# Kernel tuning notes

Hardware: AMD Instinct MI355X
Metric: run time of the kernel (lower is better)

Reference implementation:

```python
import jax, jax.numpy as jnp
import numpy as np
from jax import lax

D_MODEL = 32
N_HEADS = 8
QS = 24       # query_shape
FLANGE = 8    # memory_flange


def _conv3x3(x, w, b=None):
    y = lax.conv_general_dilated(x, w, (1, 1), 'SAME',
                                 dimension_numbers=('NCHW', 'OIHW', 'NCHW'))
    if b is not None:
        y = y + b[None, :, None, None]
    return y


def _forward(x, q_w, q_b, k_w, k_b, v_w, v_b, out_w):
    B, Cin, H, W0 = x.shape
    nh, dm, qs, fl = N_HEADS, D_MODEL, QS, FLANGE
    c = dm // nh  # depth per head (=4)

    q = _conv3x3(x, q_w, q_b)
    k = _conv3x3(x, k_w, k_b)
    v = _conv3x3(x, v_w, v_b)

    pad = (-W0) % qs
    if pad:
        p = ((0, 0), (0, 0), (0, 0), (0, pad))
        q = jnp.pad(q, p); k = jnp.pad(k, p); v = jnp.pad(v, p)
    T = q.shape[-1]
    M = T // qs
    F = 2 * fl + qs  # window length (=40)

    q = q.reshape(B, nh, c, H, T) * (c ** -0.5)
    k = jnp.pad(k.reshape(B, nh, c, H, T), ((0, 0),) * 4 + ((fl, fl),))
    v = jnp.pad(v.reshape(B, nh, c, H, T), ((0, 0),) * 4 + ((fl, fl),))

    # Faithful reproduction of torch.as_strided(k, shape, unfold_q.stride()):
    # the source uses q's (contiguous, time-length T) strides on k/v whose
    # storage rows have length T+2*fl, so we gather by storage-linear index.
    s0, s1, s2, s3 = nh * c * H * T, c * H * T, H * T, T
    idx = (jnp.arange(B)[:, None, None, None, None, None] * s0
           + jnp.arange(nh)[:, None, None, None, None] * s1
           + jnp.arange(c)[:, None, None, None] * s2
           + jnp.arange(H)[:, None, None] * s3
           + jnp.arange(M)[:, None] * qs
           + jnp.arange(F))  # (B,nh,c,H,M,F)
    uk = k.reshape(-1)[idx]
    uv = v.reshape(-1)[idx]

    qq = q.reshape(B, nh, c, H, M, qs).transpose(0, 1, 4, 3, 5, 2)
    qq = qq.reshape(B * nh * M, H * qs, c)                     # (G, H*qs, c)
    k2 = uk.transpose(0, 1, 4, 2, 3, 5).reshape(B * nh * M, c, H * F)
    v2 = uv.transpose(0, 1, 4, 3, 5, 2).reshape(B * nh * M, H * F, c)

    # note: source uses -1e-09 (not -1e9); reproduced exactly
    bias = (jnp.sum(jnp.abs(k2), axis=-2, keepdims=True) == 0).astype(k2.dtype) * (-1e-09)
    weights = jax.nn.softmax(qq @ k2 + bias, axis=-1)
    o = weights @ v2                                            # (G, H*qs, c)

    o = o.reshape(B, nh, M, H, qs, c).transpose(0, 1, 5, 3, 2, 4)
    o = o.reshape(B, dm, H, M * qs)[..., :H, :W0]
    return _conv3x3(o, out_w)


def setup_inputs() -> dict:
    key = jax.random.key(0)
    ks = jax.random.split(key, 8)
    B, Cin, H, W = 2, 64, 32, 192
    s = 0.05
    return {
        'x': jax.random.normal(ks[0], (B, Cin, H, W), jnp.float32),
        'q_w': jax.random.normal(ks[1], (D_MODEL, Cin, 3, 3), jnp.float32) * s,
        'q_b': jax.random.normal(ks[2], (D_MODEL,), jnp.float32) * s,
        'k_w': jax.random.normal(ks[3], (D_MODEL, Cin, 3, 3), jnp.float32) * s,
        'k_b': jax.random.normal(ks[4], (D_MODEL,), jnp.float32) * s,
        'v_w': jax.random.normal(ks[5], (D_MODEL, Cin, 3, 3), jnp.float32) * s,
        'v_b': jax.random.normal(ks[6], (D_MODEL,), jnp.float32) * s,
        'out_w': jax.random.normal(ks[7], (64, D_MODEL, 3, 3), jnp.float32) * s,
    }


def reference(x, q_w, q_b, k_w, k_b, v_w, v_b, out_w):
    return _forward(x, q_w, q_b, k_w, k_b, v_w, v_b, out_w)
```

## Files before the change

kernel.cpp:

```cpp
#include <hip/hip_runtime.h>

namespace {
constexpr int B   = 2;
constexpr int CIN = 64;
constexpr int H   = 32;
constexpr int W   = 192;
constexpr int DM  = 32;
constexpr int NH  = 8;
constexpr int C   = 4;
constexpr int QS  = 24;
constexpr int FL  = 8;
constexpr int T   = 192;
constexpr int TP  = T + 2 * FL;
constexpr int M   = T / QS;
constexpr int F   = 2 * FL + QS;
constexpr int HF  = H * F;
constexpr int JC  = HF / 4;
constexpr int WP  = 196;
constexpr int HWP = H * WP;

constexpr size_t XP_OFF  = 0;
constexpr size_t KVI_OFF = 0;
constexpr size_t Q_OFF   = 1310720;
constexpr size_t K_OFF   = Q_OFF + 393216;
constexpr size_t V_OFF   = K_OFF + 425984;
constexpr size_t O_OFF   = K_OFF;
constexpr size_t ZR_OFF  = V_OFF + 425984;

constexpr int S0 = NH * C * H * T;
constexpr int S1 = C * H * T;
constexpr int S2 = H * T;
constexpr int S3 = T;
}

__global__ __launch_bounds__(256) void prep_k(const float* __restrict__ x,
                                              float* __restrict__ ws) {
  int bid = blockIdx.x;
  int tid = threadIdx.x;
  if (bid < 4096) {
    if (tid < WP) {
      float v = (tid >= 1 && tid <= W) ? x[(size_t)bid * W + (tid - 1)] : 0.f;
      ws[XP_OFF + (size_t)bid * WP + tid] = v;
    }
  } else if (bid < 4224) {
    int t = (bid - 4096) * 256 + tid;
    int row = t >> 4;
    int p = t & 15;
    int col = (p < 8) ? p : (192 + p);
    size_t addr = (size_t)row * TP + col;
    ws[K_OFF + addr] = 0.f;
    ws[V_OFF + addr] = 0.f;
  } else {
    ws[ZR_OFF + tid] = 0.f;
  }
}

__global__ __launch_bounds__(192) void qkv_conv_k(
    const float* __restrict__ qw, const float* __restrict__ qb,
    const float* __restrict__ kw, const float* __restrict__ kb,
    const float* __restrict__ vw, const float* __restrict__ vb,
    float* __restrict__ ws) {
  int bid = blockIdx.x;
  int yq = bid & 7;
  int co = (bid >> 3) & 31;
  int b  = bid >> 8;
  int tid = threadIdx.x;
  int yl = tid / 48;
  int xq = tid - yl * 48;
  int y  = yq * 4 + yl;
  int xp = xq * 4;

  const float* zr  = ws + ZR_OFF;
  const float* xpb = ws + XP_OFF + (size_t)b * CIN * HWP;

  const float* p0 = (y > 0)     ? xpb + (y - 1) * WP + xp : zr + xp;
  const float* p1 = xpb + y * WP + xp;
  const float* p2 = (y < H - 1) ? xpb + (y + 1) * WP + xp : zr + xp;
  int st0 = (y > 0)     ? HWP : 0;
  int st2 = (y < H - 1) ? HWP : 0;

  const float* wq = qw + co * (CIN * 9);
  const float* wk = kw + co * (CIN * 9);
  const float* wv = vw + co * (CIN * 9);

  float q0b = qb[co], k0b = kb[co], v0b = vb[co];
  float Aq[4] = {q0b, q0b, q0b, q0b};
  float Ak[4] = {k0b, k0b, k0b, k0b};
  float Av[4] = {v0b, v0b, v0b, v0b};

#pragma unroll 2
  for (int ci = 0; ci < CIN; ++ci) {
    float4 a4 = *reinterpret_cast<const float4*>(p0);
    float2 a2 = *reinterpret_cast<const float2*>(p0 + 4);
    float4 b4 = *reinterpret_cast<const float4*>(p1);
    float2 b2 = *reinterpret_cast<const float2*>(p1 + 4);
    float4 c4 = *reinterpret_cast<const float4*>(p2);
    float2 c2 = *reinterpret_cast<const float2*>(p2 + 4);
    float av_[6] = {a4.x, a4.y, a4.z, a4.w, a2.x, a2.y};
    float bv_[6] = {b4.x, b4.y, b4.z, b4.w, b2.x, b2.y};
    float cv_[6] = {c4.x, c4.y, c4.z, c4.w, c2.x, c2.y};
#pragma unroll
    for (int dx = 0; dx < 3; ++dx) {
      float wq0 = wq[dx], wq1 = wq[3 + dx], wq2 = wq[6 + dx];
      float wk0 = wk[dx], wk1 = wk[3 + dx], wk2 = wk[6 + dx];
      float wv0 = wv[dx], wv1 = wv[3 + dx], wv2 = wv[6 + dx];
#pragma unroll
      for (int o = 0; o < 4; ++o) {
        float xa = av_[o + dx], xb = bv_[o + dx], xc = cv_[o + dx];
        Aq[o] = fmaf(xa, wq0, Aq[o]); Aq[o] = fmaf(xb, wq1, Aq[o]); Aq[o] = fmaf(xc, wq2, Aq[o]);
        Ak[o] = fmaf(xa, wk0, Ak[o]); Ak[o] = fmaf(xb, wk1, Ak[o]); Ak[o] = fmaf(xc, wk2, Ak[o]);
        Av[o] = fmaf(xa, wv0, Av[o]); Av[o] = fmaf(xb, wv1, Av[o]); Av[o] = fmaf(xc, wv2, Av[o]);
      }
    }
    p0 += st0; p1 += HWP; p2 += st2;
    wq += 9; wk += 9; wv += 9;
  }

  *reinterpret_cast<float4*>(ws + Q_OFF + ((size_t)(b * DM + co) * H + y) * T + xp) =
      make_float4(Aq[0], Aq[1], Aq[2], Aq[3]);
  int h = co >> 2, c4i = co & 3;
  size_t pa = ((size_t)((b * NH + h) * C + c4i) * H + y) * TP + FL + xp;
  *reinterpret_cast<float4*>(ws + K_OFF + pa) = make_float4(Ak[0], Ak[1], Ak[2], Ak[3]);
  *reinterpret_cast<float4*>(ws + V_OFF + pa) = make_float4(Av[0], Av[1], Av[2], Av[3]);
}

__global__ __launch_bounds__(256) void build_kv_k(float* __restrict__ ws) {
  const float* kp = ws + K_OFF;
  const float* vp = ws + V_OFF;
  float* kvi = ws + KVI_OFF;
  int t = blockIdx.x * 256 + threadIdx.x;
  int c  = t & 7;
  int gj = t >> 3;
  int g  = gj / HF;
  int j  = gj - g * HF;
  int b = g >> 6, h = (g >> 3) & 7, m = g & 7;
  int hh = j / F, f = j - hh * F;
  int ci = c & 3;
  const float* src = (c < 4) ? kp : vp;
  int addr = b * S0 + h * S1 + ci * S2 + hh * S3 + m * QS + f;
  kvi[t] = src[addr];
}

__global__ __launch_bounds__(256) void attn_k(float* __restrict__ ws) {
  const float* qbuf = ws + Q_OFF;
  const float* kvi  = ws + KVI_OFF;
  float*       ob   = ws + O_OFF;

  int g  = blockIdx.x;
  int rb = blockIdx.y;
  int b = g >> 6, h = (g >> 3) & 7, m = g & 7;
  int tid = threadIdx.x;
  int row = tid & 63;
  int jc  = __builtin_amdgcn_readfirstlane(tid >> 6);

  int r  = rb * 64 + row;
  int hh = r / QS, qi = r - hh * QS;
  size_t qidx = (((size_t)(b * DM + h * C) * H + hh) * T) + m * QS + qi;
  float q0 = qbuf[qidx]             * 0.5f;
  float q1 = qbuf[qidx + H * T]     * 0.5f;
  float q2 = qbuf[qidx + 2 * H * T] * 0.5f;
  float q3 = qbuf[qidx + 3 * H * T] * 0.5f;

  const float* kvp = kvi + ((size_t)g * HF + (size_t)jc * JC) * 8;

  float s = 0.f, o0 = 0.f, o1 = 0.f, o2 = 0.f, o3 = 0.f;
#pragma unroll 4
  for (int j = 0; j < JC; ++j) {
    float4 k4 = *reinterpret_cast<const float4*>(kvp + j * 8);
    float4 v4 = *reinterpret_cast<const float4*>(kvp + j * 8 + 4);
    float l = fmaf(q0, k4.x, fmaf(q1, k4.y, fmaf(q2, k4.z, q3 * k4.w)));
    float e = __expf(l);
    s += e;
    o0 = fmaf(e, v4.x, o0);
    o1 = fmaf(e, v4.y, o1);
    o2 = fmaf(e, v4.z, o2);
    o3 = fmaf(e, v4.w, o3);
  }

  __shared__ float red[4][64][5];
  red[jc][row][0] = s;
  red[jc][row][1] = o0;
  red[jc][row][2] = o1;
  red[jc][row][3] = o2;
  red[jc][row][4] = o3;
  __syncthreads();

  if (tid < 64) {
    float S = 0.f, O0 = 0.f, O1 = 0.f, O2 = 0.f, O3 = 0.f;
#pragma unroll
    for (int cx = 0; cx < 4; ++cx) {
      S  += red[cx][tid][0];
      O0 += red[cx][tid][1];
      O1 += red[cx][tid][2];
      O2 += red[cx][tid][3];
      O3 += red[cx][tid][4];
    }
    float inv = 1.0f / S;
    size_t obase = (((size_t)(b * DM + h * C) * H + hh) * WP) + 1 + m * QS + qi;
    ob[obase]            = O0 * inv;
    ob[obase + HWP]      = O1 * inv;
    ob[obase + 2 * HWP]  = O2 * inv;
    ob[obase + 3 * HWP]  = O3 * inv;
    if (m == 0 && qi == 0) {
      ob[obase - 1] = 0.f; ob[obase - 1 + HWP] = 0.f;
      ob[obase - 1 + 2 * HWP] = 0.f; ob[obase - 1 + 3 * HWP] = 0.f;
    }
    if (m == M - 1 && qi == QS - 1) {
      ob[obase + 1] = 0.f; ob[obase + 1 + HWP] = 0.f;
      ob[obase + 1 + 2 * HWP] = 0.f; ob[obase + 1 + 3 * HWP] = 0.f;
    }
  }
}

__global__ __launch_bounds__(192) void out_conv_k(const float* __restrict__ ws,
                                                  const float* __restrict__ ow,
                                                  float* __restrict__ out) {
  int bid = blockIdx.x;
  int yq = bid & 7;
  int cp = (bid >> 3) & 31;
  int b  = bid >> 8;
  int tid = threadIdx.x;
  int yl = tid / 48;
  int xq = tid - yl * 48;
  int y  = yq * 4 + yl;
  int xp = xq * 4;

  const float* zr  = ws + ZR_OFF;
  const float* obb = ws + O_OFF + (size_t)b * DM * HWP;

  const float* p0 = (y > 0)     ? obb + (y - 1) * WP + xp : zr + xp;
  const float* p1 = obb + y * WP + xp;
  const float* p2 = (y < H - 1) ? obb + (y + 1) * WP + xp : zr + xp;
  int st0 = (y > 0)     ? HWP : 0;
  int st2 = (y < H - 1) ? HWP : 0;

  int co0 = cp * 2;
  const float* w0 = ow + (size_t)co0 * (DM * 9);
  const float* w1 = w0 + DM * 9;
  float A0[4] = {0.f, 0.f, 0.f, 0.f};
  float A1[4] = {0.f, 0.f, 0.f, 0.f};

#pragma unroll 2
  for (int ci = 0; ci < DM; ++ci) {
    float4 a4 = *reinterpret_cast<const float4*>(p0);
    float2 a2 = *reinterpret_cast<const float2*>(p0 + 4);
    float4 b4 = *reinterpret_cast<const float4*>(p1);
    float2 b2 = *reinterpret_cast<const float2*>(p1 + 4);
    float4 c4 = *reinterpret_cast<const float4*>(p2);
    float2 c2 = *reinterpret_cast<const float2*>(p2 + 4);
    float av_[6] = {a4.x, a4.y, a4.z, a4.w, a2.x, a2.y};
    float bv_[6] = {b4.x, b4.y, b4.z, b4.w, b2.x, b2.y};
    float cv_[6] = {c4.x, c4.y, c4.z, c4.w, c2.x, c2.y};
#pragma unroll
    for (int dx = 0; dx < 3; ++dx) {
      float u0 = w0[dx], u1 = w0[3 + dx], u2 = w0[6 + dx];
      float t0 = w1[dx], t1 = w1[3 + dx], t2 = w1[6 + dx];
#pragma unroll
      for (int o = 0; o < 4; ++o) {
        float xa = av_[o + dx], xb = bv_[o + dx], xc = cv_[o + dx];
        A0[o] = fmaf(xa, u0, A0[o]); A0[o] = fmaf(xb, u1, A0[o]); A0[o] = fmaf(xc, u2, A0[o]);
        A1[o] = fmaf(xa, t0, A1[o]); A1[o] = fmaf(xb, t1, A1[o]); A1[o] = fmaf(xc, t2, A1[o]);
      }
    }
    p0 += st0; p1 += HWP; p2 += st2;
    w0 += 9; w1 += 9;
  }

  size_t ob0 = ((size_t)(b * 64 + co0) * H + y) * W + xp;
  *reinterpret_cast<float4*>(out + ob0)         = make_float4(A0[0], A0[1], A0[2], A0[3]);
  *reinterpret_cast<float4*>(out + ob0 + H * W) = make_float4(A1[0], A1[1], A1[2], A1[3]);
}

extern "C" void kernel_launch(void* const* d_in, const int* in_sizes, int n_in,
                              void* d_out, int out_size, void* d_ws, size_t ws_size,
                              hipStream_t stream) {
  const float* x  = (const float*)d_in[0];
  const float* qw = (const float*)d_in[1];
  const float* qb = (const float*)d_in[2];
  const float* kw = (const float*)d_in[3];
  const float* kb = (const float*)d_in[4];
  const float* vw = (const float*)d_in[5];
  const float* vb = (const float*)d_in[6];
  const float* ow = (const float*)d_in[7];
  float* out = (float*)d_out;
  float* ws  = (float*)d_ws;

  hipLaunchKernelGGL(prep_k,     dim3(4225), dim3(256), 0, stream, x, ws);
  hipLaunchKernelGGL(qkv_conv_k, dim3(512),  dim3(192), 0, stream,
                     qw, qb, kw, kb, vw, vb, ws);
  hipLaunchKernelGGL(build_kv_k, dim3(5120), dim3(256), 0, stream, ws);
  hipLaunchKernelGGL(attn_k,     dim3(128, 12), dim3(256), 0, stream, ws);
  hipLaunchKernelGGL(out_conv_k, dim3(512),  dim3(192), 0, stream, ws, ow, out);
}
```

Baseline: 100.3 us.

## Compute attention logits with fp16 MFMA and repack Q/K/V layouts

Replaces the scalar per-thread QK dot products with 16x16x32 fp16 MFMA instructions. Q and K are packed into fp16 tiles by new pack kernels, and V is stored transposed per channel in fp32. The cross-wave shared-memory reduction is removed; partial sums are instead combined with cross-lane shuffles inside each wave. The cost is an extra launch and fp16 rounding of logits. The MFMA input is mostly zero-padded, because only a depth of 4 is used out of 32.

```diff
diff --git a/kernel.cpp b/kernel.cpp
--- a/kernel.cpp
+++ b/kernel.cpp
@@ -1,4 +1,8 @@
 #include <hip/hip_runtime.h>
+
+typedef _Float16 f16;
+typedef __attribute__((ext_vector_type(8))) _Float16 f16x8;
+typedef __attribute__((ext_vector_type(4))) float f32x4;
 
 namespace {
 constexpr int B   = 2;
@@ -15,22 +19,29 @@
 constexpr int M   = T / QS;
 constexpr int F   = 2 * FL + QS;
 constexpr int HF  = H * F;
-constexpr int JC  = HF / 4;
 constexpr int WP  = 196;
 constexpr int HWP = H * WP;
 
-constexpr size_t XP_OFF  = 0;
-constexpr size_t KVI_OFF = 0;
-constexpr size_t Q_OFF   = 1310720;
-constexpr size_t K_OFF   = Q_OFF + 393216;
-constexpr size_t V_OFF   = K_OFF + 425984;
-constexpr size_t O_OFF   = K_OFF;
-constexpr size_t ZR_OFF  = V_OFF + 425984;
+constexpr size_t KVIK_OFF = 0;
+constexpr size_t QT_OFF   = 327680;
+constexpr size_t VT_OFF   = 524288;
+constexpr size_t XP_OFF   = 0;
+constexpr size_t Q_OFF    = 802816;
+constexpr size_t K_OFF    = 1196032;
+constexpr size_t V_OFF    = 1622016;
+constexpr size_t O_OFF    = K_OFF;
+constexpr size_t ZR_OFF   = 2048000;
 
 constexpr int S0 = NH * C * H * T;
 constexpr int S1 = C * H * T;
 constexpr int S2 = H * T;
 constexpr int S3 = T;
+}
+
+__device__ inline unsigned pk16rn(float a, float b) {
+  union { f16 h[2]; unsigned u; } c;
+  c.h[0] = (f16)a; c.h[1] = (f16)b;
+  return c.u;
 }
 
 __global__ __launch_bounds__(256) void prep_k(const float* __restrict__ x,
@@ -124,92 +135,115 @@
   *reinterpret_cast<float4*>(ws + V_OFF + pa) = make_float4(Av[0], Av[1], Av[2], Av[3]);
 }
 
-__global__ __launch_bounds__(256) void build_kv_k(float* __restrict__ ws) {
+__global__ __launch_bounds__(256) void pack_q_k(float* __restrict__ ws) {
+  int t = blockIdx.x * 256 + threadIdx.x;
+  int g = t / 768, row = t - g * 768;
+  int b = g >> 6, h = (g >> 3) & 7, m = g & 7;
+  int hh = row / QS, qi = row - hh * QS;
+  const float* qb = ws + Q_OFF;
+  size_t qidx = ((size_t)(b * DM + h * C) * H + hh) * T + m * QS + qi;
+  const float SC = 0.5f;
+  uint2 o;
+  o.x = pk16rn(qb[qidx] * SC,             qb[qidx + H * T] * SC);
+  o.y = pk16rn(qb[qidx + 2 * H * T] * SC, qb[qidx + 3 * H * T] * SC);
+  reinterpret_cast<uint2*>(ws + QT_OFF)[t] = o;
+}
+
+__global__ __launch_bounds__(256) void pack_kv_k(float* __restrict__ ws) {
+  int t = blockIdx.x * 256 + threadIdx.x;
+  int g = t / HF, key = t - g * HF;
+  int b = g >> 6, h = (g >> 3) & 7, m = g & 7;
+  int hh = key / F, f = key - hh * F;
+  int base = b * S0 + h * S1 + hh * S3 + m * QS + f;
   const float* kp = ws + K_OFF;
   const float* vp = ws + V_OFF;
-  float* kvi = ws + KVI_OFF;
-  int t = blockIdx.x * 256 + threadIdx.x;
-  int c  = t & 7;
-  int gj = t >> 3;
-  int g  = gj / HF;
-  int j  = gj - g * HF;
+  float k0 = kp[base], k1 = kp[base + S2], k2 = kp[base + 2 * S2], k3 = kp[base + 3 * S2];
+  float v0 = vp[base], v1 = vp[base + S2], v2 = vp[base + 2 * S2], v3 = vp[base + 3 * S2];
+  uint2 o; o.x = pk16rn(k0, k1); o.y = pk16rn(k2, k3);
+  reinterpret_cast<uint2*>(ws + KVIK_OFF)[t] = o;
+  float* vt = ws + VT_OFF;
+  size_t vg = (size_t)g * 4 * HF;
+  vt[vg + key]          = v0;
+  vt[vg + HF + key]     = v1;
+  vt[vg + 2 * HF + key] = v2;
+  vt[vg + 3 * HF + key] = v3;
+}
+
+__global__ __launch_bounds__(256) void attn_k(float* __restrict__ ws) {
+  const uint2* kvik = reinterpret_cast<const uint2*>(ws + KVIK_OFF);
+  const uint2* qt   = reinterpret_cast<const uint2*>(ws + QT_OFF);
+  const float* vt   = ws + VT_OFF;
+  float* ob = ws + O_OFF;
+
+  int g   = blockIdx.x;
+  int rb  = blockIdx.y;
   int b = g >> 6, h = (g >> 3) & 7, m = g & 7;
-  int hh = j / F, f = j - hh * F;
-  int ci = c & 3;
-  const float* src = (c < 4) ? kp : vp;
-  int addr = b * S0 + h * S1 + ci * S2 + hh * S3 + m * QS + f;
-  kvi[t] = src[addr];
-}
-
-__global__ __launch_bounds__(256) void attn_k(float* __restrict__ ws) {
-  const float* qbuf = ws + Q_OFF;
-  const float* kvi  = ws + KVI_OFF;
-  float*       ob   = ws + O_OFF;
-
-  int g  = blockIdx.x;
-  int rb = blockIdx.y;
-  int b = g >> 6, h = (g >> 3) & 7, m = g & 7;
-  int tid = threadIdx.x;
-  int row = tid & 63;
-  int jc  = __builtin_amdgcn_readfirstlane(tid >> 6);
-
-  int r  = rb * 64 + row;
-  int hh = r / QS, qi = r - hh * QS;
-  size_t qidx = (((size_t)(b * DM + h * C) * H + hh) * T) + m * QS + qi;
-  float q0 = qbuf[qidx]             * 0.5f;
-  float q1 = qbuf[qidx + H * T]     * 0.5f;
-  float q2 = qbuf[qidx + 2 * H * T] * 0.5f;
-  float q3 = qbuf[qidx + 3 * H * T] * 0.5f;
-
-  const float* kvp = kvi + ((size_t)g * HF + (size_t)jc * JC) * 8;
-
-  float s = 0.f, o0 = 0.f, o1 = 0.f, o2 = 0.f, o3 = 0.f;
-#pragma unroll 4
-  for (int j = 0; j < JC; ++j) {
-    float4 k4 = *reinterpret_cast<const float4*>(kvp + j * 8);
-    float4 v4 = *reinterpret_cast<const float4*>(kvp + j * 8 + 4);
-    float l = fmaf(q0, k4.x, fmaf(q1, k4.y, fmaf(q2, k4.z, q3 * k4.w)));
-    float e = __expf(l);
-    s += e;
-    o0 = fmaf(e, v4.x, o0);
-    o1 = fmaf(e, v4.y, o1);
-    o2 = fmaf(e, v4.z, o2);
-    o3 = fmaf(e, v4.w, o3);
+  int tid  = threadIdx.x;
+  int lane = tid & 63;
+  int wid  = tid >> 6;
+  int rt   = rb * 4 + wid;
+  int l15  = lane & 15;
+  int q2   = lane >> 4;
+
+  union F8 { f16x8 h; unsigned u[4]; uint2 d[2]; };
+
+  F8 qf; qf.d[0] = make_uint2(0, 0); qf.d[1] = make_uint2(0, 0);
+  if (q2 == 0) qf.d[0] = qt[(size_t)g * 768 + rt * 16 + l15];
+
+  const uint2*  kbase = kvik + (size_t)g * HF;
+  const float4* v0 = reinterpret_cast<const float4*>(vt + ((size_t)g * 4 + 0) * HF);
+  const float4* v1 = reinterpret_cast<const float4*>(vt + ((size_t)g * 4 + 1) * HF);
+  const float4* v2 = reinterpret_cast<const float4*>(vt + ((size_t)g * 4 + 2) * HF);
+  const float4* v3 = reinterpret_cast<const float4*>(vt + ((size_t)g * 4 + 3) * HF);
+
+  f32x4 z4 = {0.f, 0.f, 0.f, 0.f};
+  float o0 = 0.f, o1 = 0.f, o2 = 0.f, o3 = 0.f, s = 0.f;
+
+  for (int kt = 0; kt < 40; ++kt) {
+    int key0 = kt * 32;
+    F8 kf1, kf2;
+    kf1.d[0] = make_uint2(0, 0); kf1.d[1] = make_uint2(0, 0);
+    kf2.d[0] = make_uint2(0, 0); kf2.d[1] = make_uint2(0, 0);
+    if (q2 == 0) {
+      kf1.d[0] = kbase[key0 + l15];
+      kf2.d[0] = kbase[key0 + 16 + l15];
+    }
+    f32x4 lg1 = __builtin_amdgcn_mfma_f32_16x16x32_f16(kf1.h, qf.h, z4, 0, 0, 0);
+    f32x4 lg2 = __builtin_amdgcn_mfma_f32_16x16x32_f16(kf2.h, qf.h, z4, 0, 0, 0);
+
+    int j1 = kt * 8 + q2;
+    int j2 = kt * 8 + 4 + q2;
+    float4 va0 = v0[j1], vb0 = v0[j2];
+    float4 va1 = v1[j1], vb1 = v1[j2];
+    float4 va2 = v2[j1], vb2 = v2[j2];
+    float4 va3 = v3[j1], vb3 = v3[j2];
+
+#pragma unroll
+    for (int r = 0; r < 4; ++r) {
+      float e1 = __expf(lg1[r]);
+      float e2 = __expf(lg2[r]);
+      s += e1 + e2;
+      o0 = fmaf(e1, (&va0.x)[r], o0); o0 = fmaf(e2, (&vb0.x)[r], o0);
+      o1 = fmaf(e1, (&va1.x)[r], o1); o1 = fmaf(e2, (&vb1.x)[r], o1);
+      o2 = fmaf(e1, (&va2.x)[r], o2); o2 = fmaf(e2, (&vb2.x)[r], o2);
+      o3 = fmaf(e1, (&va3.x)[r], o3); o3 = fmaf(e2, (&vb3.x)[r], o3);
+    }
   }
 
-  __shared__ float red[4][64][5];
-  red[jc][row][0] = s;
-  red[jc][row][1] = o0;
-  red[jc][row][2] = o1;
-  red[jc][row][3] = o2;
-  red[jc][row][4] = o3;
-  __syncthreads();
-
-  if (tid < 64) {
-    float S = 0.f, O0 = 0.f, O1 = 0.f, O2 = 0.f, O3 = 0.f;
-#pragma unroll
-    for (int cx = 0; cx < 4; ++cx) {
-      S  += red[cx][tid][0];
-      O0 += red[cx][tid][1];
-      O1 += red[cx][tid][2];
-      O2 += red[cx][tid][3];
-      O3 += red[cx][tid][4];
-    }
-    float inv = 1.0f / S;
-    size_t obase = (((size_t)(b * DM + h * C) * H + hh) * WP) + 1 + m * QS + qi;
-    ob[obase]            = O0 * inv;
-    ob[obase + HWP]      = O1 * inv;
-    ob[obase + 2 * HWP]  = O2 * inv;
-    ob[obase + 3 * HWP]  = O3 * inv;
-    if (m == 0 && qi == 0) {
-      ob[obase - 1] = 0.f; ob[obase - 1 + HWP] = 0.f;
-      ob[obase - 1 + 2 * HWP] = 0.f; ob[obase - 1 + 3 * HWP] = 0.f;
-    }
-    if (m == M - 1 && qi == QS - 1) {
-      ob[obase + 1] = 0.f; ob[obase + 1 + HWP] = 0.f;
-      ob[obase + 1 + 2 * HWP] = 0.f; ob[obase + 1 + 3 * HWP] = 0.f;
-    }
-  }
+  o0 += __shfl_xor(o0, 16); o0 += __shfl_xor(o0, 32);
+  o1 += __shfl_xor(o1, 16); o1 += __shfl_xor(o1, 32);
+  o2 += __shfl_xor(o2, 16); o2 += __shfl_xor(o2, 32);
+  o3 += __shfl_xor(o3, 16); o3 += __shfl_xor(o3, 32);
+  s  += __shfl_xor(s, 16);  s  += __shfl_xor(s, 32);
+
+  float oc = (q2 == 0) ? o0 : (q2 == 1) ? o1 : (q2 == 2) ? o2 : o3;
+  float ov = oc / s;
+  int row = rt * 16 + l15;
+  int hh = row / QS, qi = row - hh * QS;
+  size_t ob_ = (((size_t)(b * DM + h * C + q2) * H + hh) * WP) + 1 + m * QS + qi;
+  ob[ob_] = ov;
+  if (m == 0 && qi == 0)          ob[ob_ - 1] = 0.f;
+  if (m == M - 1 && qi == QS - 1) ob[ob_ + 1] = 0.f;
 }
 
 __global__ __launch_bounds__(192) void out_conv_k(const float* __restrict__ ws,
@@ -288,7 +322,8 @@
   hipLaunchKernelGGL(prep_k,     dim3(4225), dim3(256), 0, stream, x, ws);
   hipLaunchKernelGGL(qkv_conv_k, dim3(512),  dim3(192), 0, stream,
                      qw, qb, kw, kb, vw, vb, ws);
-  hipLaunchKernelGGL(build_kv_k, dim3(5120), dim3(256), 0, stream, ws);
+  hipLaunchKernelGGL(pack_q_k,   dim3(384),  dim3(256), 0, stream, ws);
+  hipLaunchKernelGGL(pack_kv_k,  dim3(640),  dim3(256), 0, stream, ws);
   hipLaunchKernelGGL(attn_k,     dim3(128, 12), dim3(256), 0, stream, ws);
   hipLaunchKernelGGL(out_conv_k, dim3(512),  dim3(192), 0, stream, ws, ow, out);
 }
```

Measured after the change: 133.8 us. +33.4%, slower.
